# Kernel tuning notes

Measured on AMD Instinct MI355X. Metric: run time of the kernel, lower is better.

Reference implementation:

```python
import jax, jax.numpy as jnp
import numpy as np
from jax.ops import segment_sum, segment_max

DIM = 64
NUM_FEAT = 14
EDGE_FEAT = 4
OUT_DIM = 16
NUM_GRAPHS = 512
NEG_SLOPE = 0.01


def _leaky(v):
    return jnp.where(v >= 0, v, NEG_SLOPE * v)


def setup_inputs() -> dict:
    key = jax.random.key(0)
    ks = jax.random.split(key, 24)
    N, E = 20000, 40000
    s = 0.1
    inp = {
        "x": jax.random.normal(ks[0], (N, NUM_FEAT), jnp.float32),
        "edge_attr": jax.random.normal(ks[1], (E, EDGE_FEAT), jnp.float32),
        "edge_index": jax.random.randint(ks[2], (2, E), 0, N, jnp.int64) if jax.config.jax_enable_x64 else jax.random.randint(ks[2], (2, E), 0, N).astype(jnp.int32),
        "batch": jnp.sort(jax.random.randint(ks[3], (N,), 0, NUM_GRAPHS)).astype(jnp.int32),
        # lin0
        "lin0_w": s * jax.random.normal(ks[4], (DIM, NUM_FEAT), jnp.float32),
        "lin0_b": s * jax.random.normal(ks[5], (DIM,), jnp.float32),
        # edge network: Linear(4,dim) -> LeakyReLU -> Linear(dim, dim*dim)
        "net_w1": s * jax.random.normal(ks[6], (DIM, EDGE_FEAT), jnp.float32),
        "net_b1": s * jax.random.normal(ks[7], (DIM,), jnp.float32),
        "net_w2": s * jax.random.normal(ks[8], (DIM * DIM, DIM), jnp.float32),
        "net_b2": s * jax.random.normal(ks[9], (DIM * DIM,), jnp.float32),
        # NNConv root weight + bias
        "root_w": s * jax.random.normal(ks[10], (DIM, DIM), jnp.float32),
        "conv_b": s * jax.random.normal(ks[11], (DIM,), jnp.float32),
        # GRU (torch gate order: r, z, n)
        "gru_w_ih": s * jax.random.normal(ks[12], (3 * DIM, DIM), jnp.float32),
        "gru_w_hh": s * jax.random.normal(ks[13], (3 * DIM, DIM), jnp.float32),
        "gru_b_ih": s * jax.random.normal(ks[14], (3 * DIM,), jnp.float32),
        "gru_b_hh": s * jax.random.normal(ks[15], (3 * DIM,), jnp.float32),
        # Set2Set LSTM (input 2*dim, hidden dim; torch gate order: i, f, g, o)
        "lstm_w_ih": s * jax.random.normal(ks[16], (4 * DIM, 2 * DIM), jnp.float32),
        "lstm_w_hh": s * jax.random.normal(ks[17], (4 * DIM, DIM), jnp.float32),
        "lstm_b_ih": s * jax.random.normal(ks[18], (4 * DIM,), jnp.float32),
        "lstm_b_hh": s * jax.random.normal(ks[19], (4 * DIM,), jnp.float32),
        # lin_out
        "lout_w": s * jax.random.normal(ks[20], (OUT_DIM, 2 * DIM), jnp.float32),
        "lout_b": s * jax.random.normal(ks[21], (OUT_DIM,), jnp.float32),
    }
    return inp


def _forward(x, edge_attr, lin0_w, lin0_b, net_w1, net_b1, net_w2, net_b2,
             root_w, conv_b, gru_w_ih, gru_w_hh, gru_b_ih, gru_b_hh,
             lstm_w_ih, lstm_w_hh, lstm_b_ih, lstm_b_hh, lout_w, lout_b,
             edge_index, batch):
    N = x.shape[0]
    src, tgt = edge_index[0], edge_index[1]

    # per-edge dim x dim weight (shared across the 6 steps; edge_attr is static)
    ew = _leaky(edge_attr @ net_w1.T + net_b1) @ net_w2.T + net_b2  # [E, dim*dim]
    ew = ew.reshape(-1, DIM, DIM)  # [E, in, out]

    deg = segment_sum(jnp.ones_like(tgt, jnp.float32), tgt, num_segments=N)
    inv_deg = 1.0 / jnp.maximum(deg, 1.0)

    out = _leaky(x @ lin0_w.T + lin0_b)  # [N, dim]
    h = out
    for _ in range(6):
        msg = jnp.einsum('ed,edo->eo', out[src], ew)  # gather + per-edge matvec
        agg = segment_sum(msg, tgt, num_segments=N) * inv_deg[:, None]  # scatter-mean
        conv = agg + out @ root_w + conv_b
        m = _leaky(conv)
        # GRU cell (seq len 1)
        gi = m @ gru_w_ih.T + gru_b_ih
        gh = h @ gru_w_hh.T + gru_b_hh
        gi_r, gi_z, gi_n = jnp.split(gi, 3, axis=-1)
        gh_r, gh_z, gh_n = jnp.split(gh, 3, axis=-1)
        r = jax.nn.sigmoid(gi_r + gh_r)
        z = jax.nn.sigmoid(gi_z + gh_z)
        n = jnp.tanh(gi_n + r * gh_n)
        h = (1.0 - z) * n + z * h
        out = h

    # Set2Set, processing_steps=1
    B = NUM_GRAPHS
    q_star = jnp.zeros((B, 2 * DIM), x.dtype)
    h_l = jnp.zeros((B, DIM), x.dtype)
    c_l = jnp.zeros((B, DIM), x.dtype)
    gates = q_star @ lstm_w_ih.T + lstm_b_ih + h_l @ lstm_w_hh.T + lstm_b_hh
    gi_, gf_, gg_, go_ = jnp.split(gates, 4, axis=-1)
    i_g = jax.nn.sigmoid(gi_)
    f_g = jax.nn.sigmoid(gf_)
    g_g = jnp.tanh(gg_)
    o_g = jax.nn.sigmoid(go_)
    c = f_g * c_l + i_g * g_g
    q = o_g * jnp.tanh(c)  # [B, dim]

    e = jnp.sum(out * q[batch], axis=-1)  # [N]
    emax = segment_max(e, batch, num_segments=B)
    emax = jnp.where(jnp.isfinite(emax), emax, 0.0)
    ex = jnp.exp(e - emax[batch])
    denom = segment_sum(ex, batch, num_segments=B)
    a = ex / jnp.maximum(denom, 1e-16)[batch]
    r_read = segment_sum(a[:, None] * out, batch, num_segments=B)  # [B, dim]
    q_star = jnp.concatenate([q, r_read], axis=-1)  # [B, 2*dim]

    return q_star @ lout_w.T + lout_b  # [B, out_dim]


def reference(x, edge_attr, edge_index, batch, lin0_w, lin0_b, net_w1, net_b1,
              net_w2, net_b2, root_w, conv_b, gru_w_ih, gru_w_hh, gru_b_ih,
              gru_b_hh, lstm_w_ih, lstm_w_hh, lstm_b_ih, lstm_b_hh, lout_w, lout_b):
    return _forward(x, edge_attr, lin0_w, lin0_b, net_w1, net_b1, net_w2, net_b2,
                    root_w, conv_b, gru_w_ih, gru_w_hh, gru_b_ih, gru_b_hh,
                    lstm_w_ih, lstm_w_hh, lstm_b_ih, lstm_b_hh, lout_w, lout_b,
                    edge_index, batch)
```

## Files before the change

kernel.cpp:

```cpp
#include <hip/hip_runtime.h>
#include <math.h>

#define DIM 64
#define NFEAT 14
#define EFEAT 4
#define ODIM 16
#define NGRAPH 512
#define NEG 0.01f
#define EBLK 128
#define DSPLIT 2

typedef _Float16 f16;
typedef _Float16 f16x8 __attribute__((ext_vector_type(8)));
typedef float f32x4 __attribute__((ext_vector_type(4)));

#define MFMA(a,b,c) __builtin_amdgcn_mfma_f32_16x16x32_f16(a,b,c,0,0,0)

__device__ __forceinline__ float leaky(float v){ return v >= 0.f ? v : NEG*v; }
__device__ __forceinline__ float sigm(float v){ return 1.f/(1.f+expf(-v)); }

__global__ void k_pack(const float* __restrict__ src, f16* __restrict__ dst, int NC, int transB){
    int i = blockIdx.x*blockDim.x + threadIdx.x;
    if (i >= NC*64) return;
    int j = i & 7, l = (i >> 3) & 63, s = (i >> 9) & 1, CT = i >> 10;
    int k = ((l >> 4) << 3) + 32*s + j;
    int c = CT*16 + (l & 15);
    float v = transB ? src[(size_t)k*NC + c] : src[(size_t)c*64 + k];
    dst[i] = (f16)v;
}

__global__ void k_hid(const float* __restrict__ ea, const float* __restrict__ w1,
                      const float* __restrict__ b1, f16* __restrict__ hid16, int E){
    int i = blockIdx.x*blockDim.x + threadIdx.x;
    if (i >= E*DIM) return;
    int e = i >> 6, k = i & 63;
    const float* a = ea + (size_t)e*EFEAT;
    const float* w = w1 + k*EFEAT;
    float v = b1[k] + a[0]*w[0] + a[1]*w[1] + a[2]*w[2] + a[3]*w[3];
    hid16[i] = (f16)leaky(v);
}

__global__ void k_deg(const int* __restrict__ ei, float* __restrict__ deg, int E){
    int e = blockIdx.x*blockDim.x + threadIdx.x;
    if (e < E) atomicAdd(&deg[ei[E + e]], 1.0f);
}

__global__ void k_invdeg(float* __restrict__ deg, int N){
    int i = blockIdx.x*blockDim.x + threadIdx.x;
    if (i < N) deg[i] = 1.0f / fmaxf(deg[i], 1.0f);
}

__global__ void k_lin0(const float* __restrict__ x, const float* __restrict__ w,
                       const float* __restrict__ b, float* __restrict__ hf,
                       f16* __restrict__ out16, int N){
    int i = blockIdx.x*blockDim.x + threadIdx.x;
    if (i >= N*DIM) return;
    int n = i >> 6, o = i & 63;
    const float* xr = x + (size_t)n*NFEAT;
    const float* wr = w + o*NFEAT;
    float v = b[o];
#pragma unroll
    for (int f = 0; f < NFEAT; ++f) v += xr[f]*wr[f];
    v = leaky(v);
    hf[i] = v; out16[i] = (f16)v;
}

__global__ __launch_bounds__(256) void k_nbias(const f16x8* __restrict__ out16v,
                                               const f16x8* __restrict__ b2f,
                                               float* __restrict__ nb, int N){
    int n0 = blockIdx.x*64;
    int tid = threadIdx.x, w = tid >> 6, l = tid & 63, li = l & 15, lh = l >> 4;
    int ar = n0 + 16*w + li;
    f16x8 a0{}, a1{};
    if (ar < N){ a0 = out16v[(size_t)ar*8 + lh]; a1 = out16v[(size_t)ar*8 + lh + 4]; }
    f32x4 z = {0.f,0.f,0.f,0.f};
#pragma unroll
    for (int ct = 0; ct < 4; ++ct){
        f32x4 p = MFMA(a0, b2f[(ct*2+0)*64 + l], z);
        p = MFMA(a1, b2f[(ct*2+1)*64 + l], p);
#pragma unroll
        for (int reg = 0; reg < 4; ++reg){
            int n = n0 + 16*w + lh*4 + reg;
            if (n < N) nb[(size_t)n*64 + ct*16 + li] = p[reg];
        }
    }
}

__global__ __launch_bounds__(256) void k_fmsg(const float* __restrict__ hf,
                                              const f16x8* __restrict__ hid16v,
                                              const f16x8* __restrict__ wpf,
                                              const float* __restrict__ nb,
                                              const int* __restrict__ ei,
                                              float* __restrict__ agg, int E){
    __shared__ f16x8 Wlds[2048];
    __shared__ f16 OsT[EBLK][36];
    __shared__ int ssrc[EBLK];
    __shared__ int stgt[EBLK];
    int tid = threadIdx.x;
    int e0 = blockIdx.x*EBLK;
    int dbase = blockIdx.y*32;
    if (tid < EBLK){
        int e = e0 + tid;
        ssrc[tid] = (e < E) ? ei[e] : -1;
        stgt[tid] = (e < E) ? ei[E + e] : -1;
    }
    __syncthreads();
    for (int i = tid; i < EBLK*32; i += 256){
        int r = i >> 5, dl = i & 31;
        int s = ssrc[r];
        OsT[r][dl] = (s >= 0) ? (f16)hf[(size_t)s*64 + dbase + dl] : (f16)0.f;
    }

    int w = tid >> 6, l = tid & 63, li = l & 15, lh = l >> 4;
    f16x8 a[2][2];
#pragma unroll
    for (int rt = 0; rt < 2; ++rt){
        int e = e0 + w*32 + rt*16 + li;
        if (e < E){
            a[rt][0] = hid16v[(size_t)e*8 + lh];
            a[rt][1] = hid16v[(size_t)e*8 + lh + 4];
        } else { a[rt][0] = f16x8{}; a[rt][1] = f16x8{}; }
    }

    f16x8 p[8];
    {
        const f16x8* src = wpf + (size_t)dbase*512;
#pragma unroll
        for (int i = 0; i < 8; ++i) p[i] = src[tid + i*256];
    }

    f32x4 acc[2][4] = {};

    for (int c = 0; c < 8; ++c){
        __syncthreads();
#pragma unroll
        for (int i = 0; i < 8; ++i) Wlds[tid + i*256] = p[i];
        __syncthreads();
        if (c < 7){
            const f16x8* src = wpf + (size_t)(dbase + (c+1)*4)*512;
#pragma unroll
            for (int i = 0; i < 8; ++i) p[i] = src[tid + i*256];
        }
#pragma unroll
        for (int dd = 0; dd < 4; ++dd){
            int dl = c*4 + dd;
            f16 s0 = OsT[w*32 + li][dl];
            f16 s1 = OsT[w*32 + 16 + li][dl];
            f16x8 as00 = a[0][0]*s0, as01 = a[0][1]*s0;
            f16x8 as10 = a[1][0]*s1, as11 = a[1][1]*s1;
#pragma unroll
            for (int ct = 0; ct < 4; ++ct){
                f16x8 b0 = Wlds[(dd*8 + ct*2 + 0)*64 + l];
                f16x8 b1 = Wlds[(dd*8 + ct*2 + 1)*64 + l];
                acc[0][ct] = MFMA(as00, b0, acc[0][ct]);
                acc[0][ct] = MFMA(as01, b1, acc[0][ct]);
                acc[1][ct] = MFMA(as10, b0, acc[1][ct]);
                acc[1][ct] = MFMA(as11, b1, acc[1][ct]);
            }
        }
    }

#pragma unroll
    for (int rt = 0; rt < 2; ++rt){
#pragma unroll
        for (int reg = 0; reg < 4; ++reg){
            int row = w*32 + rt*16 + lh*4 + reg;
            int t = stgt[row];
            if (t < 0) continue;
            int s = ssrc[row];
#pragma unroll
            for (int ct = 0; ct < 4; ++ct){
                int col = ct*16 + li;
                float v = acc[rt][ct][reg];
                if (blockIdx.y == 0) v += nb[(size_t)s*64 + col];
                atomicAdd(&agg[(size_t)t*64 + col], v);
            }
        }
    }
}

__global__ __launch_bounds__(256) void k_node(float* __restrict__ hf,
                                              f16* __restrict__ out16,
                                              const f16x8* __restrict__ out16v,
                                              float* __restrict__ agg,
                                              const float* __restrict__ invdeg,
                                              const float* __restrict__ convb,
                                              const f16x8* __restrict__ wrf,
                                              const f16x8* __restrict__ wihf,
                                              const f16x8* __restrict__ whhf,
                                              const float* __restrict__ bih,
                                              const float* __restrict__ bhh,
                                              const f16x8* __restrict__ b2f,
                                              float* __restrict__ nb, int N){
    __shared__ f16 Ms[64][72];
    int n0 = blockIdx.x*64;
    int tid = threadIdx.x, w = tid >> 6, l = tid & 63, li = l & 15, lh = l >> 4;
    f32x4 z = {0.f,0.f,0.f,0.f};

    int ar = n0 + 16*w + li;
    f16x8 a0{}, a1{};
    if (ar < N){ a0 = out16v[(size_t)ar*8 + lh]; a1 = out16v[(size_t)ar*8 + lh + 4]; }

    int nrow[4]; float invd[4];
#pragma unroll
    for (int reg = 0; reg < 4; ++reg){
        nrow[reg] = n0 + 16*w + lh*4 + reg;
        invd[reg] = (nrow[reg] < N) ? invdeg[nrow[reg]] : 0.f;
    }

#pragma unroll
    for (int ct = 0; ct < 4; ++ct){
        f32x4 p = MFMA(a0, wrf[(ct*2+0)*64 + l], z);
        p = MFMA(a1, wrf[(ct*2+1)*64 + l], p);
        int col = ct*16 + li;
        float cb = convb[col];
#pragma unroll
        for (int reg = 0; reg < 4; ++reg){
            int n = nrow[reg];
            float m = 0.f;
            if (n < N){
                size_t idx = (size_t)n*64 + col;
                m = leaky(p[reg] + agg[idx]*invd[reg] + cb);
                agg[idx] = 0.f;
            }
            Ms[16*w + lh*4 + reg][col] = (f16)m;
        }
    }

    f16x8 am0 = *(const f16x8*)&Ms[16*w + li][lh*8];
    f16x8 am1 = *(const f16x8*)&Ms[16*w + li][lh*8 + 32];

#pragma unroll
    for (int ctq = 0; ctq < 4; ++ctq){
        int col = ctq*16 + li;
        f32x4 pir = MFMA(am0, wihf[((ctq+0)*2+0)*64 + l], z);
        pir = MFMA(am1, wihf[((ctq+0)*2+1)*64 + l], pir);
        f32x4 piz = MFMA(am0, wihf[((ctq+4)*2+0)*64 + l], z);
        piz = MFMA(am1, wihf[((ctq+4)*2+1)*64 + l], piz);
        f32x4 pin = MFMA(am0, wihf[((ctq+8)*2+0)*64 + l], z);
        pin = MFMA(am1, wihf[((ctq+8)*2+1)*64 + l], pin);
        f32x4 phr = MFMA(a0, whhf[((ctq+0)*2+0)*64 + l], z);
        phr = MFMA(a1, whhf[((ctq+0)*2+1)*64 + l], phr);
        f32x4 phz = MFMA(a0, whhf[((ctq+4)*2+0)*64 + l], z);
        phz = MFMA(a1, whhf[((ctq+4)*2+1)*64 + l], phz);
        f32x4 phn = MFMA(a0, whhf[((ctq+8)*2+0)*64 + l], z);
        phn = MFMA(a1, whhf[((ctq+8)*2+1)*64 + l], phn);
        float bir = bih[col], biz = bih[64+col], bin = bih[128+col];
        float bhr = bhh[col], bhz = bhh[64+col], bhn = bhh[128+col];
#pragma unroll
        for (int reg = 0; reg < 4; ++reg){
            int n = nrow[reg];
            float hnew = 0.f;
            if (n < N){
                float hv = hf[(size_t)n*64 + col];
                float r  = sigm(pir[reg] + bir + phr[reg] + bhr);
                float zz = sigm(piz[reg] + biz + phz[reg] + bhz);
                float nn = tanhf(pin[reg] + bin + r*(phn[reg] + bhn));
                hnew = (1.f - zz)*nn + zz*hv;
                hf[(size_t)n*64 + col] = hnew;
                out16[(size_t)n*64 + col] = (f16)hnew;
            }
            Ms[16*w + lh*4 + reg][col] = (f16)hnew;
        }
    }

    f16x8 an0 = *(const f16x8*)&Ms[16*w + li][lh*8];
    f16x8 an1 = *(const f16x8*)&Ms[16*w + li][lh*8 + 32];
#pragma unroll
    for (int ct = 0; ct < 4; ++ct){
        f32x4 p = MFMA(an0, b2f[(ct*2+0)*64 + l], z);
        p = MFMA(an1, b2f[(ct*2+1)*64 + l], p);
#pragma unroll
        for (int reg = 0; reg < 4; ++reg){
            int n = nrow[reg];
            if (n < N) nb[(size_t)n*64 + ct*16 + li] = p[reg];
        }
    }
}

__global__ void k_q(const float* __restrict__ bih, const float* __restrict__ bhh,
                    float* __restrict__ q){
    int j = threadIdx.x;
    if (j >= 64) return;
    float gi = bih[j]       + bhh[j];
    float gg = bih[128+j]   + bhh[128+j];
    float go = bih[192+j]   + bhh[192+j];
    float c = sigm(gi)*tanhf(gg);
    q[j] = sigm(go)*tanhf(c);
}

__device__ __forceinline__ unsigned fkey(float f){
    unsigned u = __float_as_uint(f);
    return (u >> 31) ? ~u : (u | 0x80000000u);
}

__global__ void k_edot(const float* __restrict__ out, const float* __restrict__ q,
                       const int* __restrict__ batch, float* __restrict__ ebuf,
                       unsigned* __restrict__ emaxk, int N){
    int gw = (blockIdx.x*blockDim.x + threadIdx.x) >> 6;
    int d = threadIdx.x & 63;
    if (gw >= N) return;
    float v = out[(size_t)gw*64 + d] * q[d];
#pragma unroll
    for (int s = 32; s; s >>= 1) v += __shfl_xor(v, s, 64);
    if (d == 0){
        ebuf[gw] = v;
        atomicMax(&emaxk[batch[gw]], fkey(v));
    }
}

__global__ void k_ex(float* __restrict__ ebuf, const unsigned* __restrict__ emaxk,
                     const int* __restrict__ batch, float* __restrict__ denom, int N){
    int n = blockIdx.x*blockDim.x + threadIdx.x;
    if (n >= N) return;
    int b = batch[n];
    unsigned k = emaxk[b];
    float em = (k == 0u) ? 0.f
             : ((k >> 31) ? __uint_as_float(k ^ 0x80000000u) : __uint_as_float(~k));
    float ex = expf(ebuf[n] - em);
    ebuf[n] = ex;
    atomicAdd(&denom[b], ex);
}

__global__ void k_rr(const float* __restrict__ out, const float* __restrict__ ebuf,
                     const float* __restrict__ denom, const int* __restrict__ batch,
                     float* __restrict__ rr, int N){
    int gw = (blockIdx.x*blockDim.x + threadIdx.x) >> 6;
    int o = threadIdx.x & 63;
    if (gw >= N) return;
    int b = batch[gw];
    float a = ebuf[gw] / fmaxf(denom[b], 1e-16f);
    atomicAdd(&rr[(size_t)b*64 + o], a * out[(size_t)gw*64 + o]);
}

__global__ void k_out(const float* __restrict__ q, const float* __restrict__ rr,
                      const float* __restrict__ lw, const float* __restrict__ lb,
                      float* __restrict__ dout){
    int i = blockIdx.x*blockDim.x + threadIdx.x;
    if (i >= NGRAPH*ODIM) return;
    int b = i / ODIM, j = i % ODIM;
    const float* w = lw + j*128;
    float acc = lb[j];
#pragma unroll 8
    for (int d = 0; d < 64; ++d) acc += w[d]*q[d];
    const float* rb = rr + (size_t)b*64;
#pragma unroll 8
    for (int d = 0; d < 64; ++d) acc += w[64+d]*rb[d];
    dout[i] = acc;
}

extern "C" void kernel_launch(void* const* d_in, const int* in_sizes, int n_in,
                              void* d_out, int out_size, void* d_ws, size_t ws_size,
                              hipStream_t stream){
    const float* x     = (const float*)d_in[0];
    const float* ea    = (const float*)d_in[1];
    const int*   ei    = (const int*)  d_in[2];
    const int*   batch = (const int*)  d_in[3];
    const float* lin0w = (const float*)d_in[4];
    const float* lin0b = (const float*)d_in[5];
    const float* w1    = (const float*)d_in[6];
    const float* b1    = (const float*)d_in[7];
    const float* w2    = (const float*)d_in[8];
    const float* b2    = (const float*)d_in[9];
    const float* rootw = (const float*)d_in[10];
    const float* convb = (const float*)d_in[11];
    const float* gwih  = (const float*)d_in[12];
    const float* gwhh  = (const float*)d_in[13];
    const float* gbih  = (const float*)d_in[14];
    const float* gbhh  = (const float*)d_in[15];
    const float* lsbih = (const float*)d_in[18];
    const float* lsbhh = (const float*)d_in[19];
    const float* loutw = (const float*)d_in[20];
    const float* loutb = (const float*)d_in[21];

    int N = in_sizes[0] / NFEAT;
    int E = in_sizes[1] / EFEAT;

    char* p = (char*)d_ws;
    size_t off = 0;
    auto carve = [&](size_t bytes) -> void* {
        void* r = p + off;
        off += (bytes + 255) & ~(size_t)255;
        return r;
    };
    f16*      hid16  = (f16*)     carve((size_t)E*64*2);
    float*    hf     = (float*)   carve((size_t)N*64*4);
    f16*      out16  = (f16*)     carve((size_t)N*64*2);
    float*    nb     = (float*)   carve((size_t)N*64*4);
    float*    qv     = (float*)   carve(64*4);
    float*    ebuf   = (float*)   carve((size_t)N*4);
    f16*      wpf    = (f16*)     carve((size_t)4096*64*2);
    f16*      wrf    = (f16*)     carve(64*64*2);
    f16*      b2f    = (f16*)     carve(64*64*2);
    f16*      wihf   = (f16*)     carve(192*64*2);
    f16*      whhf   = (f16*)     carve(192*64*2);
    size_t zero_beg = off;
    float*    agg    = (float*)   carve((size_t)N*64*4);
    float*    invdeg = (float*)   carve((size_t)N*4);
    unsigned* emaxk  = (unsigned*)carve(NGRAPH*4);
    float*    denom  = (float*)   carve(NGRAPH*4);
    float*    rr     = (float*)   carve((size_t)NGRAPH*64*4);
    size_t zero_end = off;

    hipMemsetAsync(p + zero_beg, 0, zero_end - zero_beg, stream);

    k_pack<<<(4096*64 + 255)/256, 256, 0, stream>>>(w2,    wpf,  4096, 0);
    k_pack<<<(64*64   + 255)/256, 256, 0, stream>>>(rootw, wrf,  64,   1);
    k_pack<<<(64*64   + 255)/256, 256, 0, stream>>>(b2,    b2f,  64,   1);
    k_pack<<<(192*64  + 255)/256, 256, 0, stream>>>(gwih,  wihf, 192,  0);
    k_pack<<<(192*64  + 255)/256, 256, 0, stream>>>(gwhh,  whhf, 192,  0);

    k_hid<<<((size_t)E*64 + 255)/256, 256, 0, stream>>>(ea, w1, b1, hid16, E);
    k_deg<<<(E + 255)/256, 256, 0, stream>>>(ei, invdeg, E);
    k_invdeg<<<(N + 255)/256, 256, 0, stream>>>(invdeg, N);
    k_lin0<<<((size_t)N*64 + 255)/256, 256, 0, stream>>>(x, lin0w, lin0b, hf, out16, N);

    int eb  = (E + EBLK - 1)/EBLK;
    int nbk = (N + 63)/64;
    int node_grid = ((size_t)N*64 + 255)/256;

    k_nbias<<<nbk, 256, 0, stream>>>((const f16x8*)out16, (const f16x8*)b2f, nb, N);
    for (int it = 0; it < 6; ++it){
        k_fmsg<<<dim3(eb, DSPLIT), 256, 0, stream>>>(hf, (const f16x8*)hid16,
                                                     (const f16x8*)wpf, nb, ei, agg, E);
        k_node<<<nbk, 256, 0, stream>>>(hf, out16, (const f16x8*)out16, agg, invdeg,
                                        convb, (const f16x8*)wrf, (const f16x8*)wihf,
                                        (const f16x8*)whhf, gbih, gbhh,
                                        (const f16x8*)b2f, nb, N);
    }

    k_q<<<1, 64, 0, stream>>>(lsbih, lsbhh, qv);
    k_edot<<<node_grid, 256, 0, stream>>>(hf, qv, batch, ebuf, emaxk, N);
    k_ex<<<(N + 255)/256, 256, 0, stream>>>(ebuf, emaxk, batch, denom, N);
    k_rr<<<node_grid, 256, 0, stream>>>(hf, ebuf, denom, batch, rr, N);
    k_out<<<(NGRAPH*ODIM + 255)/256, 256, 0, stream>>>(qv, rr, loutw, loutb, (float*)d_out);
}
```

Before: 496.8 us.

## Restructure edge message kernel to contract hidden first then scale by source features

The NNConv message kernel is reorganised. It now computes per-edge products of the hidden edge vector with W2 slices through MFMA, then multiplies by the fp32 source features on vector ALUs, instead of pre-scaling the fp16 hidden vector by the source feature before each MFMA. The grid is split 8 ways (4 output-column quarters times 2 input halves), with a whole 32-row weight slice loaded into LDS once and no per-chunk reload. Separately, the five pack kernels are fused into one, k_q is folded into k_invdeg, and zeroing of agg moves into k_lin0 to cut launches and memset size. The new path adds more MFMA work per edge, more redundant hf gathers, and extra FMA work on vector ALUs.

New measurement: 1.470 ms. +195.8%, slower.

```diff
diff --git a/kernel.cpp b/kernel.cpp
--- a/kernel.cpp
+++ b/kernel.cpp
@@ -7,8 +7,7 @@
 #define ODIM 16
 #define NGRAPH 512
 #define NEG 0.01f
-#define EBLK 128
-#define DSPLIT 2
+#define EBLK 256
 
 typedef _Float16 f16;
 typedef _Float16 f16x8 __attribute__((ext_vector_type(8)));
@@ -19,14 +18,31 @@
 __device__ __forceinline__ float leaky(float v){ return v >= 0.f ? v : NEG*v; }
 __device__ __forceinline__ float sigm(float v){ return 1.f/(1.f+expf(-v)); }
 
-__global__ void k_pack(const float* __restrict__ src, f16* __restrict__ dst, int NC, int transB){
-    int i = blockIdx.x*blockDim.x + threadIdx.x;
-    if (i >= NC*64) return;
+__device__ __forceinline__ void pack_one(const float* __restrict__ src, f16* __restrict__ dst,
+                                         int NC, int transB, int i){
     int j = i & 7, l = (i >> 3) & 63, s = (i >> 9) & 1, CT = i >> 10;
     int k = ((l >> 4) << 3) + 32*s + j;
     int c = CT*16 + (l & 15);
     float v = transB ? src[(size_t)k*NC + c] : src[(size_t)c*64 + k];
     dst[i] = (f16)v;
+}
+
+__global__ void k_packall(const float* __restrict__ w2, const float* __restrict__ rootw,
+                          const float* __restrict__ b2, const float* __restrict__ gwih,
+                          const float* __restrict__ gwhh,
+                          f16* __restrict__ wpf, f16* __restrict__ wrf,
+                          f16* __restrict__ b2f, f16* __restrict__ wihf,
+                          f16* __restrict__ whhf){
+    int i = blockIdx.x*256 + threadIdx.x;
+    if (i < 262144){ pack_one(w2, wpf, 4096, 0, i); return; }
+    i -= 262144;
+    if (i < 4096){ pack_one(rootw, wrf, 64, 1, i); return; }
+    i -= 4096;
+    if (i < 4096){ pack_one(b2, b2f, 64, 1, i); return; }
+    i -= 4096;
+    if (i < 12288){ pack_one(gwih, wihf, 192, 0, i); return; }
+    i -= 12288;
+    if (i < 12288){ pack_one(gwhh, whhf, 192, 0, i); return; }
 }
 
 __global__ void k_hid(const float* __restrict__ ea, const float* __restrict__ w1,
@@ -45,14 +61,23 @@
     if (e < E) atomicAdd(&deg[ei[E + e]], 1.0f);
 }
 
-__global__ void k_invdeg(float* __restrict__ deg, int N){
+__global__ void k_invdeg(float* __restrict__ deg, const float* __restrict__ bih,
+                         const float* __restrict__ bhh, float* __restrict__ q, int N){
     int i = blockIdx.x*blockDim.x + threadIdx.x;
     if (i < N) deg[i] = 1.0f / fmaxf(deg[i], 1.0f);
+    if (blockIdx.x == 0 && threadIdx.x < 64){
+        int j = threadIdx.x;
+        float gi = bih[j]     + bhh[j];
+        float gg = bih[128+j] + bhh[128+j];
+        float go = bih[192+j] + bhh[192+j];
+        float c = sigm(gi)*tanhf(gg);
+        q[j] = sigm(go)*tanhf(c);
+    }
 }
 
 __global__ void k_lin0(const float* __restrict__ x, const float* __restrict__ w,
                        const float* __restrict__ b, float* __restrict__ hf,
-                       f16* __restrict__ out16, int N){
+                       f16* __restrict__ out16, float* __restrict__ agg, int N){
     int i = blockIdx.x*blockDim.x + threadIdx.x;
     if (i >= N*DIM) return;
     int n = i >> 6, o = i & 63;
@@ -62,7 +87,7 @@
 #pragma unroll
     for (int f = 0; f < NFEAT; ++f) v += xr[f]*wr[f];
     v = leaky(v);
-    hf[i] = v; out16[i] = (f16)v;
+    hf[i] = v; out16[i] = (f16)v; agg[i] = 0.f;
 }
 
 __global__ __launch_bounds__(256) void k_nbias(const f16x8* __restrict__ out16v,
@@ -92,89 +117,72 @@
                                               const float* __restrict__ nb,
                                               const int* __restrict__ ei,
                                               float* __restrict__ agg, int E){
-    __shared__ f16x8 Wlds[2048];
-    __shared__ f16 OsT[EBLK][36];
-    __shared__ int ssrc[EBLK];
-    __shared__ int stgt[EBLK];
+    __shared__ f16x8 Wlds[4096];
     int tid = threadIdx.x;
     int e0 = blockIdx.x*EBLK;
-    int dbase = blockIdx.y*32;
-    if (tid < EBLK){
-        int e = e0 + tid;
-        ssrc[tid] = (e < E) ? ei[e] : -1;
-        stgt[tid] = (e < E) ? ei[E + e] : -1;
+    int oh = blockIdx.y & 3;
+    int dh = blockIdx.y >> 2;
+    int dbase = dh*32;
+    for (int i = tid; i < 4096; i += 256){
+        int l = i & 63, s = (i >> 6) & 1, dl = i >> 7;
+        Wlds[i] = wpf[((size_t)(dbase + dl)*8 + oh*2 + s)*64 + l];
+    }
+
+    int w = tid >> 6, l = tid & 63, li = l & 15, lh = l >> 4;
+    int sa[4], ta[4];
+    f16x8 b[4][2];
+#pragma unroll
+    for (int rt = 0; rt < 4; ++rt){
+        int e = e0 + w*64 + rt*16 + li;
+        sa[rt] = (e < E) ? ei[e] : -1;
+        ta[rt] = (e < E) ? ei[E + e] : -1;
+        if (e < E){
+            b[rt][0] = hid16v[(size_t)e*8 + lh];
+            b[rt][1] = hid16v[(size_t)e*8 + lh + 4];
+        } else { b[rt][0] = f16x8{}; b[rt][1] = f16x8{}; }
     }
     __syncthreads();
-    for (int i = tid; i < EBLK*32; i += 256){
-        int r = i >> 5, dl = i & 31;
-        int s = ssrc[r];
-        OsT[r][dl] = (s >= 0) ? (f16)hf[(size_t)s*64 + dbase + dl] : (f16)0.f;
-    }
-
-    int w = tid >> 6, l = tid & 63, li = l & 15, lh = l >> 4;
-    f16x8 a[2][2];
-#pragma unroll
-    for (int rt = 0; rt < 2; ++rt){
-        int e = e0 + w*32 + rt*16 + li;
-        if (e < E){
-            a[rt][0] = hid16v[(size_t)e*8 + lh];
-            a[rt][1] = hid16v[(size_t)e*8 + lh + 4];
-        } else { a[rt][0] = f16x8{}; a[rt][1] = f16x8{}; }
-    }
-
-    f16x8 p[8];
-    {
-        const f16x8* src = wpf + (size_t)dbase*512;
-#pragma unroll
-        for (int i = 0; i < 8; ++i) p[i] = src[tid + i*256];
-    }
-
-    f32x4 acc[2][4] = {};
-
-    for (int c = 0; c < 8; ++c){
-        __syncthreads();
-#pragma unroll
-        for (int i = 0; i < 8; ++i) Wlds[tid + i*256] = p[i];
-        __syncthreads();
-        if (c < 7){
-            const f16x8* src = wpf + (size_t)(dbase + (c+1)*4)*512;
-#pragma unroll
-            for (int i = 0; i < 8; ++i) p[i] = src[tid + i*256];
-        }
-#pragma unroll
-        for (int dd = 0; dd < 4; ++dd){
-            int dl = c*4 + dd;
-            f16 s0 = OsT[w*32 + li][dl];
-            f16 s1 = OsT[w*32 + 16 + li][dl];
-            f16x8 as00 = a[0][0]*s0, as01 = a[0][1]*s0;
-            f16x8 as10 = a[1][0]*s1, as11 = a[1][1]*s1;
-#pragma unroll
-            for (int ct = 0; ct < 4; ++ct){
-                f16x8 b0 = Wlds[(dd*8 + ct*2 + 0)*64 + l];
-                f16x8 b1 = Wlds[(dd*8 + ct*2 + 1)*64 + l];
-                acc[0][ct] = MFMA(as00, b0, acc[0][ct]);
-                acc[0][ct] = MFMA(as01, b1, acc[0][ct]);
-                acc[1][ct] = MFMA(as10, b0, acc[1][ct]);
-                acc[1][ct] = MFMA(as11, b1, acc[1][ct]);
+
+    const float4* hf4 = (const float4*)hf;
+    f32x4 acc[4] = {};
+    const f32x4 z = {0.f,0.f,0.f,0.f};
+
+#pragma unroll
+    for (int q = 0; q < 2; ++q){
+        float os[4][16];
+#pragma unroll
+        for (int rt = 0; rt < 4; ++rt){
+#pragma unroll
+            for (int j = 0; j < 4; ++j){
+                float4 v = make_float4(0.f,0.f,0.f,0.f);
+                if (sa[rt] >= 0) v = hf4[(size_t)sa[rt]*16 + dh*8 + q*4 + j];
+                os[rt][j*4+0]=v.x; os[rt][j*4+1]=v.y; os[rt][j*4+2]=v.z; os[rt][j*4+3]=v.w;
             }
         }
-    }
-
-#pragma unroll
-    for (int rt = 0; rt < 2; ++rt){
+#pragma unroll
+        for (int dd = 0; dd < 16; ++dd){
+            const int dl = q*16 + dd;
+            f16x8 A0 = Wlds[(dl*2+0)*64 + l];
+            f16x8 A1 = Wlds[(dl*2+1)*64 + l];
+#pragma unroll
+            for (int rt = 0; rt < 4; ++rt){
+                f32x4 p = MFMA(A0, b[rt][0], z);
+                p = MFMA(A1, b[rt][1], p);
+#pragma unroll
+                for (int i = 0; i < 4; ++i) acc[rt][i] += os[rt][dd]*p[i];
+            }
+        }
+    }
+
+#pragma unroll
+    for (int rt = 0; rt < 4; ++rt){
+        if (ta[rt] < 0) continue;
 #pragma unroll
         for (int reg = 0; reg < 4; ++reg){
-            int row = w*32 + rt*16 + lh*4 + reg;
-            int t = stgt[row];
-            if (t < 0) continue;
-            int s = ssrc[row];
-#pragma unroll
-            for (int ct = 0; ct < 4; ++ct){
-                int col = ct*16 + li;
-                float v = acc[rt][ct][reg];
-                if (blockIdx.y == 0) v += nb[(size_t)s*64 + col];
-                atomicAdd(&agg[(size_t)t*64 + col], v);
-            }
+            int col = oh*16 + lh*4 + reg;
+            float v = acc[rt][reg];
+            if (dh == 0) v += nb[(size_t)sa[rt]*64 + col];
+            atomicAdd(&agg[(size_t)ta[rt]*64 + col], v);
         }
     }
 }
@@ -276,17 +284,6 @@
             if (n < N) nb[(size_t)n*64 + ct*16 + li] = p[reg];
         }
     }
-}
-
-__global__ void k_q(const float* __restrict__ bih, const float* __restrict__ bhh,
-                    float* __restrict__ q){
-    int j = threadIdx.x;
-    if (j >= 64) return;
-    float gi = bih[j]       + bhh[j];
-    float gg = bih[128+j]   + bhh[128+j];
-    float go = bih[192+j]   + bhh[192+j];
-    float c = sigm(gi)*tanhf(gg);
-    q[j] = sigm(go)*tanhf(c);
 }
 
 __device__ __forceinline__ unsigned fkey(float f){
@@ -387,6 +384,7 @@
     float*    hf     = (float*)   carve((size_t)N*64*4);
     f16*      out16  = (f16*)     carve((size_t)N*64*2);
     float*    nb     = (float*)   carve((size_t)N*64*4);
+    float*    agg    = (float*)   carve((size_t)N*64*4);
     float*    qv     = (float*)   carve(64*4);
     float*    ebuf   = (float*)   carve((size_t)N*4);
     f16*      wpf    = (f16*)     carve((size_t)4096*64*2);
@@ -395,7 +393,6 @@
     f16*      wihf   = (f16*)     carve(192*64*2);
     f16*      whhf   = (f16*)     carve(192*64*2);
     size_t zero_beg = off;
-    float*    agg    = (float*)   carve((size_t)N*64*4);
     float*    invdeg = (float*)   carve((size_t)N*4);
     unsigned* emaxk  = (unsigned*)carve(NGRAPH*4);
     float*    denom  = (float*)   carve(NGRAPH*4);
@@ -404,16 +401,13 @@
 
     hipMemsetAsync(p + zero_beg, 0, zero_end - zero_beg, stream);
 
-    k_pack<<<(4096*64 + 255)/256, 256, 0, stream>>>(w2,    wpf,  4096, 0);
-    k_pack<<<(64*64   + 255)/256, 256, 0, stream>>>(rootw, wrf,  64,   1);
-    k_pack<<<(64*64   + 255)/256, 256, 0, stream>>>(b2,    b2f,  64,   1);
-    k_pack<<<(192*64  + 255)/256, 256, 0, stream>>>(gwih,  wihf, 192,  0);
-    k_pack<<<(192*64  + 255)/256, 256, 0, stream>>>(gwhh,  whhf, 192,  0);
-
+    int pack_total = 262144 + 4096 + 4096 + 12288 + 12288;
+    k_packall<<<(pack_total + 255)/256, 256, 0, stream>>>(w2, rootw, b2, gwih, gwhh,
+                                                          wpf, wrf, b2f, wihf, whhf);
     k_hid<<<((size_t)E*64 + 255)/256, 256, 0, stream>>>(ea, w1, b1, hid16, E);
     k_deg<<<(E + 255)/256, 256, 0, stream>>>(ei, invdeg, E);
-    k_invdeg<<<(N + 255)/256, 256, 0, stream>>>(invdeg, N);
-    k_lin0<<<((size_t)N*64 + 255)/256, 256, 0, stream>>>(x, lin0w, lin0b, hf, out16, N);
+    k_invdeg<<<(N + 255)/256, 256, 0, stream>>>(invdeg, lsbih, lsbhh, qv, N);
+    k_lin0<<<((size_t)N*64 + 255)/256, 256, 0, stream>>>(x, lin0w, lin0b, hf, out16, agg, N);
 
     int eb  = (E + EBLK - 1)/EBLK;
     int nbk = (N + 63)/64;
@@ -421,15 +415,14 @@
 
     k_nbias<<<nbk, 256, 0, stream>>>((const f16x8*)out16, (const f16x8*)b2f, nb, N);
     for (int it = 0; it < 6; ++it){
-        k_fmsg<<<dim3(eb, DSPLIT), 256, 0, stream>>>(hf, (const f16x8*)hid16,
-                                                     (const f16x8*)wpf, nb, ei, agg, E);
+        k_fmsg<<<dim3(eb, 8), 256, 0, stream>>>(hf, (const f16x8*)hid16,
+                                                (const f16x8*)wpf, nb, ei, agg, E);
         k_node<<<nbk, 256, 0, stream>>>(hf, out16, (const f16x8*)out16, agg, invdeg,
                                         convb, (const f16x8*)wrf, (const f16x8*)wihf,
                                         (const f16x8*)whhf, gbih, gbhh,
                                         (const f16x8*)b2f, nb, N);
     }
 
-    k_q<<<1, 64, 0, stream>>>(lsbih, lsbhh, qv);
     k_edot<<<node_grid, 256, 0, stream>>>(hf, qv, batch, ebuf, emaxk, N);
     k_ex<<<(N + 255)/256, 256, 0, stream>>>(ebuf, emaxk, batch, denom, N);
     k_rr<<<node_grid, 256, 0, stream>>>(hf, ebuf, denom, batch, rr, N);
```
